# Kernel tuning notes

Measured on AMD Instinct MI355X. Metric: run time of the kernel, lower is better.

## Reference

```python
import jax, jax.numpy as jnp
import numpy as np


def setup_inputs() -> dict:
    key = jax.random.key(0)
    k1, k2, k3, k4 = jax.random.split(key, 4)
    n_entity, n_rel, dim = 2048, 32, 512
    entities = jax.random.normal(k1, (n_entity, dim), dtype=jnp.float32)
    relations = jax.random.normal(k2, (n_rel, dim), dtype=jnp.float32)
    W = jax.random.normal(k3, (dim, dim), dtype=jnp.float32) * (1.0 / np.sqrt(dim))
    b = jax.random.normal(k4, (dim,), dtype=jnp.float32) * 0.01
    return {"entities": entities, "relations": relations, "W": W, "b": b}


def reference(entities, relations, W, b):
    # gate_nn applied to both entities and relations (shared Linear)
    E = entities @ W.T + b            # [n_entity, dim]
    R = relations @ W.T + b           # [n_rel, dim]
    # Diagonal RESCAL: scores[e, r, f] = sum_d E[e,d] * R[r,d] * E[f,d]
    # Equivalent to the per-relation loop E @ diag(R_r) @ E^T, fused into one einsum.
    scores = jnp.einsum('ed,rd,fd->erf', E, R, E)  # [n_entity, n_rel, n_entity]
    return scores
```

## Files before the change

kernel.cpp:

```cpp
#include <hip/hip_runtime.h>

typedef __attribute__((ext_vector_type(8))) __bf16 bf16x8;
typedef __attribute__((ext_vector_type(4))) float f32x4;

__device__ __forceinline__ float bf2f(unsigned int u) {
    return __uint_as_float(u << 16);
}
__device__ __forceinline__ unsigned short f2bf(float f) {
    unsigned int x = __float_as_uint(f);
    return (unsigned short)((x + 0x7fffu + ((x >> 16) & 1u)) >> 16);
}

__global__ void cast_f32_bf16(const float* __restrict__ in,
                              unsigned short* __restrict__ out, int n4) {
    int i = blockIdx.x * blockDim.x + threadIdx.x;
    if (i >= n4) return;
    float4 v = reinterpret_cast<const float4*>(in)[i];
    ushort4 o;
    o.x = f2bf(v.x); o.y = f2bf(v.y); o.z = f2bf(v.z); o.w = f2bf(v.w);
    reinterpret_cast<ushort4*>(out)[i] = o;
}

__device__ __forceinline__ unsigned int mul2bf(unsigned int a, unsigned int b) {
    float a0 = bf2f(a & 0xffffu), a1 = bf2f(a >> 16);
    float b0 = bf2f(b & 0xffffu), b1 = bf2f(b >> 16);
    return (unsigned int)f2bf(a0 * b0) | ((unsigned int)f2bf(a1 * b1) << 16);
}

__global__ void build_ap(const unsigned short* __restrict__ G,
                         unsigned short* __restrict__ Ap) {
    int t = blockIdx.x * blockDim.x + threadIdx.x;
    int row = t >> 6;
    int d = (t & 63) * 8;
    int e = row >> 5, r = row & 31;
    const uint4 ev = *reinterpret_cast<const uint4*>(G + e * 512 + d);
    const uint4 rv = *reinterpret_cast<const uint4*>(G + (2048 + r) * 512 + d);
    uint4 o;
    o.x = mul2bf(ev.x, rv.x);
    o.y = mul2bf(ev.y, rv.y);
    o.z = mul2bf(ev.z, rv.z);
    o.w = mul2bf(ev.w, rv.w);
    *reinterpret_cast<uint4*>(Ap + (size_t)row * 512 + d) = o;
}

#define BM 128
#define BN 128
#define BK 64

template <bool GUARD_M, bool BIAS_BF16OUT>
__global__ __launch_bounds__(256, 2) void mfma_gemm_bt(
    const unsigned short* __restrict__ A,
    const unsigned short* __restrict__ Bt,
    const float* __restrict__ bias,
    void* __restrict__ Cout,
    int M, int N, int K) {
    __shared__ __align__(16) unsigned short As[BM * BK];
    __shared__ __align__(16) unsigned short Bs[BN * BK];

    const int tid = threadIdx.x;
    const int lane = tid & 63;
    const int wave = tid >> 6;
    const int nbn = N / BN;
    const int bm0 = (blockIdx.x / nbn) * BM;
    const int bn0 = (blockIdx.x % nbn) * BN;
    const int wr = wave >> 1, wc = wave & 1;

    f32x4 acc[4][4] = {};

    const int srow = wave * 32 + (lane >> 3);
    const int scol = (lane & 7) * 8;

    for (int kb = 0; kb < K; kb += BK) {
#pragma unroll
        for (int i = 0; i < 4; ++i) {
            int row = bm0 + srow + i * 8;
            if (GUARD_M) row = min(row, M - 1);
            const unsigned short* src = A + (size_t)row * K + kb + scol;
            unsigned short* dst = &As[(wave * 32 + i * 8) * BK];
            __builtin_amdgcn_global_load_lds(
                (const __attribute__((address_space(1))) void*)src,
                (__attribute__((address_space(3))) void*)dst, 16, 0, 0);
        }
#pragma unroll
        for (int i = 0; i < 4; ++i) {
            int row = bn0 + srow + i * 8;
            const unsigned short* src = Bt + (size_t)row * K + kb + scol;
            unsigned short* dst = &Bs[(wave * 32 + i * 8) * BK];
            __builtin_amdgcn_global_load_lds(
                (const __attribute__((address_space(1))) void*)src,
                (__attribute__((address_space(3))) void*)dst, 16, 0, 0);
        }
        __syncthreads();

#pragma unroll
        for (int ks = 0; ks < BK / 32; ++ks) {
            const int k0 = ks * 32 + (lane >> 4) * 8;
            bf16x8 av[4], bv[4];
#pragma unroll
            for (int m = 0; m < 4; ++m)
                av[m] = *reinterpret_cast<const bf16x8*>(
                    &As[(wr * 64 + m * 16 + (lane & 15)) * BK + k0]);
#pragma unroll
            for (int n = 0; n < 4; ++n)
                bv[n] = *reinterpret_cast<const bf16x8*>(
                    &Bs[(wc * 64 + n * 16 + (lane & 15)) * BK + k0]);
#pragma unroll
            for (int m = 0; m < 4; ++m)
#pragma unroll
                for (int n = 0; n < 4; ++n)
                    acc[m][n] = __builtin_amdgcn_mfma_f32_16x16x32_bf16(
                        av[m], bv[n], acc[m][n], 0, 0, 0);
        }
        __syncthreads();
    }

#pragma unroll
    for (int m = 0; m < 4; ++m) {
#pragma unroll
        for (int n = 0; n < 4; ++n) {
#pragma unroll
            for (int j = 0; j < 4; ++j) {
                int row = bm0 + wr * 64 + m * 16 + (lane >> 4) * 4 + j;
                int col = bn0 + wc * 64 + n * 16 + (lane & 15);
                if (GUARD_M && row >= M) continue;
                float v = acc[m][n][j];
                if (BIAS_BF16OUT) {
                    v += bias[col];
                    ((unsigned short*)Cout)[(size_t)row * N + col] = f2bf(v);
                } else {
                    ((float*)Cout)[(size_t)row * N + col] = v;
                }
            }
        }
    }
}

#define NT8 8

__global__ __launch_bounds__(512, 2) void gemm256_8ph(
    const unsigned short* __restrict__ A,
    const unsigned short* __restrict__ B,
    float* __restrict__ C) {
    __shared__ __align__(16) unsigned short lds[65536];

    const int tid = threadIdx.x;
    const int lane = tid & 63;
    const int wave = tid >> 6;
    const int wr = wave >> 2;
    const int wc = wave & 3;
    const int laneM = lane & 15;
    const int laneK = (lane >> 4) * 8;
    const int kx = (lane & 7) * 8;

    const int swz = (blockIdx.x & 7) * 256 + (blockIdx.x >> 3);
    const int bm0 = (swz >> 3) * 256;
    const int bn0 = (swz & 7) * 256;

    const int sr0 = tid >> 3;
    const int sc = ((tid & 7) * 8) ^ (((tid >> 3) & 7) * 8);

    auto STAGE = [&](const unsigned short* mat, int row0, int kb, int slotOff) {
#pragma unroll
        for (int rd = 0; rd < 2; ++rd) {
            const unsigned short* src = mat + (size_t)(row0 + sr0 + rd * 64) * 512 + kb + sc;
            unsigned short* dst = &lds[slotOff + wave * 512 + rd * 4096];
            __builtin_amdgcn_global_load_lds(
                (const __attribute__((address_space(1))) void*)src,
                (__attribute__((address_space(3))) void*)dst, 16, 0, 0);
        }
    };
    auto RD = [&](int slotOff, int r, int ks) -> bf16x8 {
        return *reinterpret_cast<const bf16x8*>(
            &lds[slotOff + r * 64 + (((ks * 32) + laneK) ^ kx)]);
    };

    f32x4 acc[8][4] = {};
    bf16x8 av[4][2], bv0[2][2], bv1[2][2];

    STAGE(A, bm0,        0, 0 * 32768 + 0 * 8192);
    STAGE(B, bn0,        0, 0 * 32768 + 16384 + 0 * 8192);
    STAGE(B, bn0 + 128,  0, 0 * 32768 + 16384 + 1 * 8192);
    STAGE(A, bm0 + 128,  0, 0 * 32768 + 1 * 8192);
    STAGE(B, bn0,       64, 1 * 32768 + 16384 + 0 * 8192);
    STAGE(A, bm0,       64, 1 * 32768 + 0 * 8192);
    STAGE(B, bn0 + 128, 64, 1 * 32768 + 16384 + 1 * 8192);
    asm volatile("s_waitcnt vmcnt(6)" ::: "memory");
    __builtin_amdgcn_s_barrier();

#pragma unroll
    for (int t = 0; t < NT8; ++t) {
        const int P = t & 1;
        const int sA = P * 32768 + wr * 8192;
        const int sB = P * 32768 + 16384 + (wc >> 1) * 8192;
        const int rB = (wc & 1) * 64;

#pragma unroll
        for (int m = 0; m < 4; ++m)
#pragma unroll
            for (int ks = 0; ks < 2; ++ks)
                av[m][ks] = RD(sA, m * 16 + laneM, ks);
#pragma unroll
        for (int n = 0; n < 2; ++n)
#pragma unroll
            for (int ks = 0; ks < 2; ++ks)
                bv0[n][ks] = RD(sB, rB + n * 16 + laneM, ks);
        if (t + 1 < NT8)
            STAGE(A, bm0 + 128, (t + 1) * 64, ((t + 1) & 1) * 32768 + 8192);
        __builtin_amdgcn_s_barrier();
        asm volatile("s_waitcnt lgkmcnt(0)" ::: "memory");
        __builtin_amdgcn_sched_barrier(0);
        __builtin_amdgcn_s_setprio(1);
#pragma unroll
        for (int ks = 0; ks < 2; ++ks)
#pragma unroll
            for (int m = 0; m < 4; ++m)
#pragma unroll
                for (int n = 0; n < 2; ++n)
                    acc[m][n] = __builtin_amdgcn_mfma_f32_16x16x32_bf16(
                        av[m][ks], bv0[n][ks], acc[m][n], 0, 0, 0);
        __builtin_amdgcn_s_setprio(0);
        __builtin_amdgcn_s_barrier();

#pragma unroll
        for (int n = 0; n < 2; ++n)
#pragma unroll
            for (int ks = 0; ks < 2; ++ks)
                bv1[n][ks] = RD(sB, rB + (2 + n) * 16 + laneM, ks);
        __builtin_amdgcn_s_barrier();
        asm volatile("s_waitcnt lgkmcnt(0)" ::: "memory");
        __builtin_amdgcn_sched_barrier(0);
        __builtin_amdgcn_s_setprio(1);
#pragma unroll
        for (int ks = 0; ks < 2; ++ks)
#pragma unroll
            for (int m = 0; m < 4; ++m)
#pragma unroll
                for (int n = 0; n < 2; ++n)
                    acc[m][2 + n] = __builtin_amdgcn_mfma_f32_16x16x32_bf16(
                        av[m][ks], bv1[n][ks], acc[m][2 + n], 0, 0, 0);
        __builtin_amdgcn_s_setprio(0);
        __builtin_amdgcn_s_barrier();

#pragma unroll
        for (int m = 0; m < 4; ++m)
#pragma unroll
            for (int ks = 0; ks < 2; ++ks)
                av[m][ks] = RD(sA, 64 + m * 16 + laneM, ks);
        if (t + 2 < NT8)
            STAGE(B, bn0, (t + 2) * 64, ((t + 2) & 1) * 32768 + 16384);
        __builtin_amdgcn_s_barrier();
        asm volatile("s_waitcnt lgkmcnt(0)" ::: "memory");
        __builtin_amdgcn_sched_barrier(0);
        __builtin_amdgcn_s_setprio(1);
#pragma unroll
        for (int ks = 0; ks < 2; ++ks)
#pragma unroll
            for (int m = 0; m < 4; ++m)
#pragma unroll
                for (int n = 0; n < 2; ++n)
                    acc[4 + m][2 + n] = __builtin_amdgcn_mfma_f32_16x16x32_bf16(
                        av[m][ks], bv1[n][ks], acc[4 + m][2 + n], 0, 0, 0);
        __builtin_amdgcn_s_setprio(0);
        __builtin_amdgcn_s_barrier();

        if (t + 2 < NT8) {
            STAGE(A, bm0, (t + 2) * 64, ((t + 2) & 1) * 32768);
            STAGE(B, bn0 + 128, (t + 2) * 64, ((t + 2) & 1) * 32768 + 16384 + 8192);
        }
        __builtin_amdgcn_s_barrier();
        __builtin_amdgcn_s_setprio(1);
#pragma unroll
        for (int ks = 0; ks < 2; ++ks)
#pragma unroll
            for (int m = 0; m < 4; ++m)
#pragma unroll
                for (int n = 0; n < 2; ++n)
                    acc[4 + m][n] = __builtin_amdgcn_mfma_f32_16x16x32_bf16(
                        av[m][ks], bv0[n][ks], acc[4 + m][n], 0, 0, 0);
        __builtin_amdgcn_s_setprio(0);
        if (t < NT8 - 1) {
            if (t == NT8 - 2)
                asm volatile("s_waitcnt vmcnt(0)" ::: "memory");
            else
                asm volatile("s_waitcnt vmcnt(6)" ::: "memory");
            __builtin_amdgcn_s_barrier();
        }
    }

#pragma unroll
    for (int mi = 0; mi < 8; ++mi)
#pragma unroll
        for (int ni = 0; ni < 4; ++ni)
#pragma unroll
            for (int j = 0; j < 4; ++j) {
                int row = bm0 + wr * 128 + mi * 16 + (lane >> 4) * 4 + j;
                int col = bn0 + wc * 64 + ni * 16 + laneM;
                C[(size_t)row * 2048 + col] = acc[mi][ni][j];
            }
}

extern "C" void kernel_launch(void* const* d_in, const int* in_sizes, int n_in,
                              void* d_out, int out_size, void* d_ws, size_t ws_size,
                              hipStream_t stream) {
    const float* entities  = (const float*)d_in[0];
    const float* relations = (const float*)d_in[1];
    const float* W         = (const float*)d_in[2];
    const float* b         = (const float*)d_in[3];

    char* ws = (char*)d_ws;
    unsigned short* W_bf = (unsigned short*)ws;
    unsigned short* X_bf = (unsigned short*)(ws + 524288);
    unsigned short* G_bf = (unsigned short*)(ws + 524288 + 2129920);
    unsigned short* Ap   = (unsigned short*)(ws + 524288 + 2129920 + 2129920);

    cast_f32_bf16<<<1024, 256, 0, stream>>>(entities, X_bf, 262144);
    cast_f32_bf16<<<16, 256, 0, stream>>>(relations, X_bf + 2048 * 512, 4096);
    cast_f32_bf16<<<256, 256, 0, stream>>>(W, W_bf, 65536);

    mfma_gemm_bt<true, true><<<17 * 4, 256, 0, stream>>>(
        X_bf, W_bf, b, (void*)G_bf, 2080, 512, 512);

    build_ap<<<16384, 256, 0, stream>>>(G_bf, Ap);

    gemm256_8ph<<<2048, 512, 0, stream>>>(Ap, G_bf, (float*)d_out);
}
```

Measured before the change: 243.2 us.

## Fuse entity-relation product into main GEMM A-operand staging

Measured after the change: 295.7 us. +21.6%, slower.

```diff
diff --git a/kernel.cpp b/kernel.cpp
--- a/kernel.cpp
+++ b/kernel.cpp
@@ -9,6 +9,18 @@
 __device__ __forceinline__ unsigned short f2bf(float f) {
     unsigned int x = __float_as_uint(f);
     return (unsigned short)((x + 0x7fffu + ((x >> 16) & 1u)) >> 16);
+}
+
+__device__ __forceinline__ unsigned int mulpack(unsigned int e, unsigned int r) {
+    float e0 = __uint_as_float(e << 16);
+    float e1 = __uint_as_float(e & 0xffff0000u);
+    float r0 = __uint_as_float(r << 16);
+    float r1 = __uint_as_float(r & 0xffff0000u);
+    float p0 = e0 * r0;
+    float p1 = e1 * r1;
+    unsigned int out;
+    asm("v_cvt_pk_bf16_f32 %0, %1, %2" : "=v"(out) : "v"(p0), "v"(p1));
+    return out;
 }
 
 __global__ void cast_f32_bf16(const float* __restrict__ in,
@@ -19,28 +31,6 @@
     ushort4 o;
     o.x = f2bf(v.x); o.y = f2bf(v.y); o.z = f2bf(v.z); o.w = f2bf(v.w);
     reinterpret_cast<ushort4*>(out)[i] = o;
-}
-
-__device__ __forceinline__ unsigned int mul2bf(unsigned int a, unsigned int b) {
-    float a0 = bf2f(a & 0xffffu), a1 = bf2f(a >> 16);
-    float b0 = bf2f(b & 0xffffu), b1 = bf2f(b >> 16);
-    return (unsigned int)f2bf(a0 * b0) | ((unsigned int)f2bf(a1 * b1) << 16);
-}
-
-__global__ void build_ap(const unsigned short* __restrict__ G,
-                         unsigned short* __restrict__ Ap) {
-    int t = blockIdx.x * blockDim.x + threadIdx.x;
-    int row = t >> 6;
-    int d = (t & 63) * 8;
-    int e = row >> 5, r = row & 31;
-    const uint4 ev = *reinterpret_cast<const uint4*>(G + e * 512 + d);
-    const uint4 rv = *reinterpret_cast<const uint4*>(G + (2048 + r) * 512 + d);
-    uint4 o;
-    o.x = mul2bf(ev.x, rv.x);
-    o.y = mul2bf(ev.y, rv.y);
-    o.z = mul2bf(ev.z, rv.z);
-    o.w = mul2bf(ev.w, rv.w);
-    *reinterpret_cast<uint4*>(Ap + (size_t)row * 512 + d) = o;
 }
 
 #define BM 128
@@ -137,9 +127,8 @@
 
 #define NT8 8
 
-__global__ __launch_bounds__(512, 2) void gemm256_8ph(
-    const unsigned short* __restrict__ A,
-    const unsigned short* __restrict__ B,
+__global__ __launch_bounds__(512, 2) void gemm256_8ph_fused(
+    const unsigned short* __restrict__ G,
     float* __restrict__ C) {
     __shared__ __align__(16) unsigned short lds[65536];
 
@@ -156,13 +145,14 @@
     const int bm0 = (swz >> 3) * 256;
     const int bn0 = (swz & 7) * 256;
 
+    const int kplain = (tid & 7) * 8;
     const int sr0 = tid >> 3;
-    const int sc = ((tid & 7) * 8) ^ (((tid >> 3) & 7) * 8);
-
-    auto STAGE = [&](const unsigned short* mat, int row0, int kb, int slotOff) {
+    const int kswz = kplain ^ ((sr0 & 7) * 8);
+
+    auto STAGE_B = [&](int row0, int kb, int slotOff) {
 #pragma unroll
         for (int rd = 0; rd < 2; ++rd) {
-            const unsigned short* src = mat + (size_t)(row0 + sr0 + rd * 64) * 512 + kb + sc;
+            const unsigned short* src = G + (size_t)(row0 + sr0 + rd * 64) * 512 + kb + kswz;
             unsigned short* dst = &lds[slotOff + wave * 512 + rd * 4096];
             __builtin_amdgcn_global_load_lds(
                 (const __attribute__((address_space(1))) void*)src,
@@ -174,17 +164,40 @@
             &lds[slotOff + r * 64 + (((ks * 32) + laneK) ^ kx)]);
     };
 
+    uint4 Eg[4], Rg[4];
+    auto ISSUE_A = [&](int kb) {
+#pragma unroll
+        for (int g = 0; g < 4; ++g) {
+            int er = bm0 + (g >> 1) * 128 + (g & 1) * 64 + sr0;
+            int e = er >> 5, r = er & 31;
+            Eg[g] = *reinterpret_cast<const uint4*>(G + (size_t)e * 512 + kb + kplain);
+            Rg[g] = *reinterpret_cast<const uint4*>(G + (size_t)(2048 + r) * 512 + kb + kplain);
+        }
+    };
+    auto WRITE_A = [&](int gbuf) {
+#pragma unroll
+        for (int g = 0; g < 4; ++g) {
+            uint4 o;
+            o.x = mulpack(Eg[g].x, Rg[g].x);
+            o.y = mulpack(Eg[g].y, Rg[g].y);
+            o.z = mulpack(Eg[g].z, Rg[g].z);
+            o.w = mulpack(Eg[g].w, Rg[g].w);
+            *reinterpret_cast<uint4*>(
+                &lds[gbuf * 32768 + (g >> 1) * 8192 + ((g & 1) * 64 + sr0) * 64 + kswz]) = o;
+        }
+    };
+
     f32x4 acc[8][4] = {};
     bf16x8 av[4][2], bv0[2][2], bv1[2][2];
 
-    STAGE(A, bm0,        0, 0 * 32768 + 0 * 8192);
-    STAGE(B, bn0,        0, 0 * 32768 + 16384 + 0 * 8192);
-    STAGE(B, bn0 + 128,  0, 0 * 32768 + 16384 + 1 * 8192);
-    STAGE(A, bm0 + 128,  0, 0 * 32768 + 1 * 8192);
-    STAGE(B, bn0,       64, 1 * 32768 + 16384 + 0 * 8192);
-    STAGE(A, bm0,       64, 1 * 32768 + 0 * 8192);
-    STAGE(B, bn0 + 128, 64, 1 * 32768 + 16384 + 1 * 8192);
-    asm volatile("s_waitcnt vmcnt(6)" ::: "memory");
+    ISSUE_A(0);
+    STAGE_B(bn0,       0, 0 * 32768 + 16384 + 0 * 8192);
+    STAGE_B(bn0 + 128, 0, 0 * 32768 + 16384 + 1 * 8192);
+    STAGE_B(bn0,      64, 1 * 32768 + 16384 + 0 * 8192);
+    STAGE_B(bn0 + 128,64, 1 * 32768 + 16384 + 1 * 8192);
+    WRITE_A(0);
+    asm volatile("s_waitcnt vmcnt(4)" ::: "memory");
+    asm volatile("s_waitcnt lgkmcnt(0)" ::: "memory");
     __builtin_amdgcn_s_barrier();
 
 #pragma unroll
@@ -205,7 +218,7 @@
             for (int ks = 0; ks < 2; ++ks)
                 bv0[n][ks] = RD(sB, rB + n * 16 + laneM, ks);
         if (t + 1 < NT8)
-            STAGE(A, bm0 + 128, (t + 1) * 64, ((t + 1) & 1) * 32768 + 8192);
+            ISSUE_A((t + 1) * 64);
         __builtin_amdgcn_s_barrier();
         asm volatile("s_waitcnt lgkmcnt(0)" ::: "memory");
         __builtin_amdgcn_sched_barrier(0);
@@ -247,7 +260,9 @@
             for (int ks = 0; ks < 2; ++ks)
                 av[m][ks] = RD(sA, 64 + m * 16 + laneM, ks);
         if (t + 2 < NT8)
-            STAGE(B, bn0, (t + 2) * 64, ((t + 2) & 1) * 32768 + 16384);
+            STAGE_B(bn0, (t + 2) * 64, ((t + 2) & 1) * 32768 + 16384);
+        if (t + 1 < NT8)
+            WRITE_A((t + 1) & 1);
         __builtin_amdgcn_s_barrier();
         asm volatile("s_waitcnt lgkmcnt(0)" ::: "memory");
         __builtin_amdgcn_sched_barrier(0);
@@ -263,10 +278,8 @@
         __builtin_amdgcn_s_setprio(0);
         __builtin_amdgcn_s_barrier();
 
-        if (t + 2 < NT8) {
-            STAGE(A, bm0, (t + 2) * 64, ((t + 2) & 1) * 32768);
-            STAGE(B, bn0 + 128, (t + 2) * 64, ((t + 2) & 1) * 32768 + 16384 + 8192);
-        }
+        if (t + 2 < NT8)
+            STAGE_B(bn0 + 128, (t + 2) * 64, ((t + 2) & 1) * 32768 + 16384 + 8192);
         __builtin_amdgcn_s_barrier();
         __builtin_amdgcn_s_setprio(1);
 #pragma unroll
@@ -282,7 +295,7 @@
             if (t == NT8 - 2)
                 asm volatile("s_waitcnt vmcnt(0)" ::: "memory");
             else
-                asm volatile("s_waitcnt vmcnt(6)" ::: "memory");
+                asm volatile("s_waitcnt vmcnt(4)" ::: "memory");
             __builtin_amdgcn_s_barrier();
         }
     }
@@ -311,7 +324,6 @@
     unsigned short* W_bf = (unsigned short*)ws;
     unsigned short* X_bf = (unsigned short*)(ws + 524288);
     unsigned short* G_bf = (unsigned short*)(ws + 524288 + 2129920);
-    unsigned short* Ap   = (unsigned short*)(ws + 524288 + 2129920 + 2129920);
 
     cast_f32_bf16<<<1024, 256, 0, stream>>>(entities, X_bf, 262144);
     cast_f32_bf16<<<16, 256, 0, stream>>>(relations, X_bf + 2048 * 512, 4096);
@@ -320,7 +332,5 @@
     mfma_gemm_bt<true, true><<<17 * 4, 256, 0, stream>>>(
         X_bf, W_bf, b, (void*)G_bf, 2080, 512, 512);
 
-    build_ap<<<16384, 256, 0, stream>>>(G_bf, Ap);
-
-    gemm256_8ph<<<2048, 512, 0, stream>>>(Ap, G_bf, (float*)d_out);
-}
+    gemm256_8ph_fused<<<2048, 512, 0, stream>>>(G_bf, (float*)d_out);
+}
```
